# Kernel optimization log

Measured on AMD Instinct MI355X. Metric: run time of the kernel, lower is better.

## Reference

```python
import jax, jax.numpy as jnp
import numpy as np

EPS = 1e-6

def rmsnorm(x, w):
    # x: (B, N, D), w: (D,)
    var = jnp.mean(jnp.square(x), axis=-1, keepdims=True)
    return x * jax.lax.rsqrt(var + EPS) * w

def head_mixing(x):
    # Parameter-free cross-head mix: split each head's D dims into N chunks
    # and transpose the (head, chunk) axes. x: (B, N, D), D % N == 0.
    B, N, D = x.shape
    c = D // N
    return x.reshape(B, N, N, c).transpose(0, 2, 1, 3).reshape(B, N, D)

def setup_inputs() -> dict:
    key = jax.random.key(0)
    ks = jax.random.split(key, 4)
    B, N, D, H = 8192, 16, 256, 512
    return {
        "x": jax.random.normal(ks[0], (B, N, D), dtype=jnp.float32),
        "norm1_w": jnp.ones((D,), dtype=jnp.float32),
        "norm2_w": jnp.ones((D,), dtype=jnp.float32),
        "w1": jax.random.normal(ks[1], (N, D, H), dtype=jnp.float32) * (1.0 / np.sqrt(D)),
        "w3": jax.random.normal(ks[2], (N, D, H), dtype=jnp.float32) * (1.0 / np.sqrt(D)),
        "w2": jax.random.normal(ks[3], (N, H, D), dtype=jnp.float32) * (1.0 / np.sqrt(H)),
    }

def reference(x, norm1_w, norm2_w, w1, w3, w2):
    # P = HeadMixing(RMSNorm(X)) + X
    p = head_mixing(rmsnorm(x, norm1_w)) + x
    # Q = PerHeadSwiGLUFFN(RMSNorm(P)) + P  (grouped per-head SwiGLU)
    pn = rmsnorm(p, norm2_w)                       # (B, N, D)
    g = jnp.einsum('bnd,ndh->bnh', pn, w1)         # gate proj
    u = jnp.einsum('bnd,ndh->bnh', pn, w3)         # up proj
    h = jax.nn.silu(g) * u                         # (B, N, H)
    q = jnp.einsum('bnh,nhd->bnd', h, w2) + p
    return q
```

## Files before the change

kernel.cpp:

```cpp
#include <hip/hip_runtime.h>
#include <hip/hip_bf16.h>

#define B_ 8192
#define N_ 16
#define D_ 256
#define H_ 512

using bf16x8 = __attribute__((ext_vector_type(8))) short;
using f32x4  = __attribute__((ext_vector_type(4))) float;

__device__ __forceinline__ void gload_lds16(const void* g, void* l) {
    __builtin_amdgcn_global_load_lds(
        (const __attribute__((address_space(1))) void*)g,
        (__attribute__((address_space(3))) void*)l, 16, 0, 0);
}

__device__ __forceinline__ short f2bf(float f) {
    unsigned int u = __float_as_uint(f);
    u += 0x7fffu + ((u >> 16) & 1u);
    return (short)(u >> 16);
}

__device__ __forceinline__ float bf2f(short s) {
    return __uint_as_float(((unsigned int)(unsigned short)s) << 16);
}

__device__ __forceinline__ unsigned int pack2(float lo, float hi) {
    return (unsigned int)(unsigned short)f2bf(lo)
         | ((unsigned int)(unsigned short)f2bf(hi) << 16);
}

__device__ __forceinline__ f32x4 mfma(bf16x8 a, bf16x8 b, f32x4 c) {
    return __builtin_amdgcn_mfma_f32_16x16x32_bf16(a, b, c, 0, 0, 0);
}

__device__ __forceinline__ bf16x8 rd64(const short* base, int row, int g) {
    int gp = (g ^ row) & 7;
    return *(const bf16x8*)&base[(row << 6) + (gp << 3)];
}

template<int NT, int SA, int SB>
__device__ __forceinline__ void gemmc(const short* __restrict__ Ag,
                                      const short* __restrict__ Bg,
                                      short* As, short* Bs,
                                      f32x4 (&acc)[4][4],
                                      int t, int rowA0, int rowB0) {
    int lane = t & 63;
    int l16 = lane & 15, kq = lane >> 4;
    int srow = t >> 3;
    int sg   = ((t & 7) ^ srow) & 7;
    const short* Asrc = Ag + (size_t)srow * SA + sg * 8;
    const short* Bsrc = Bg + (size_t)srow * SB + sg * 8;

#pragma unroll
    for (int kt = 0; kt < NT; ++kt) {
        const int k0 = kt * 64;
#pragma unroll
        for (int rnd = 0; rnd < 4; ++rnd)
            gload_lds16(Asrc + rnd * 32 * SA + k0, As + rnd * 2048 + t * 8);
#pragma unroll
        for (int rnd = 0; rnd < 4; ++rnd)
            gload_lds16(Bsrc + rnd * 32 * SB + k0, Bs + rnd * 2048 + t * 8);
        __syncthreads();

#pragma unroll
        for (int kh = 0; kh < 2; ++kh) {
            int g = kh * 4 + kq;
            bf16x8 aF[4], bF[4];
#pragma unroll
            for (int j = 0; j < 4; ++j)
                bF[j] = rd64(Bs, rowB0 + j * 16 + l16, g);
#pragma unroll
            for (int i = 0; i < 4; ++i)
                aF[i] = rd64(As, rowA0 + i * 16 + l16, g);
#pragma unroll
            for (int i = 0; i < 4; ++i)
#pragma unroll
                for (int j = 0; j < 4; ++j)
                    acc[i][j] = mfma(aF[i], bF[j], acc[i][j]);
        }
        __syncthreads();
    }
}

__global__ __launch_bounds__(256) void k_prep(const float* __restrict__ w1,
                                              const float* __restrict__ w3,
                                              const float* __restrict__ w2,
                                              short* __restrict__ wgu,
                                              short* __restrict__ w2t) {
    int o = blockIdx.x * 256 + threadIdx.x;
    int n = o >> 17;
    int r = o & 131071;
    int h = r >> 8, d = r & 255;
    size_t base = ((size_t)n * 1024 + (h >> 4) * 32 + (h & 15)) * 256 + d;
    wgu[base]            = f2bf(w1[(size_t)n * 131072 + (size_t)d * 512 + h]);
    wgu[base + 16 * 256] = f2bf(w3[(size_t)n * 131072 + (size_t)d * 512 + h]);
    int d2 = r >> 9, h2 = r & 511;
    w2t[o] = f2bf(w2[(size_t)n * 131072 + (size_t)h2 * 256 + d2]);
}

__global__ __launch_bounds__(256) void k_mix(const float* __restrict__ x,
                                             const float* __restrict__ n1w,
                                             const float* __restrict__ n2w,
                                             unsigned int* __restrict__ pb_u,
                                             unsigned int* __restrict__ pn_u) {
    __shared__ __align__(16) float xs[N_ * D_];
    __shared__ __align__(16) float ps[N_ * D_];
    __shared__ float inv1[N_];
    __shared__ float inv2[N_];
    int b = blockIdx.x;
    int t = threadIdx.x;
    int w = t >> 6, lane = t & 63;

    const float4* xb4 = (const float4*)(x + (size_t)b * (N_ * D_));
    float4* xs4 = (float4*)xs;
    float4* ps4 = (float4*)ps;
#pragma unroll
    for (int i = 0; i < 4; ++i) xs4[t + i * 256] = xb4[t + i * 256];
    __syncthreads();

#pragma unroll
    for (int q = 0; q < 4; ++q) {
        int row = w * 4 + q;
        float4 v = xs4[row * 64 + lane];
        float s = v.x * v.x + v.y * v.y + v.z * v.z + v.w * v.w;
        s += __shfl_xor(s, 1);  s += __shfl_xor(s, 2);
        s += __shfl_xor(s, 4);  s += __shfl_xor(s, 8);
        s += __shfl_xor(s, 16); s += __shfl_xor(s, 32);
        if (lane == 0) inv1[row] = rsqrtf(s * (1.0f / 256.0f) + 1e-6f);
    }
    __syncthreads();

    {
        int n = t >> 4, j = t & 15;
        float i1 = inv1[n];
#pragma unroll 1
        for (int m = 0; m < 16; ++m) {
            int mm = (m + n) & 15;
            float v = xs[n * 256 + mm * 16 + j] * i1 * n1w[mm * 16 + j]
                    + xs[mm * 256 + t];
            ps[mm * 256 + t] = v;
        }
    }
    __syncthreads();

#pragma unroll
    for (int q = 0; q < 4; ++q) {
        int row = w * 4 + q;
        float4 v = ps4[row * 64 + lane];
        float s = v.x * v.x + v.y * v.y + v.z * v.z + v.w * v.w;
        s += __shfl_xor(s, 1);  s += __shfl_xor(s, 2);
        s += __shfl_xor(s, 4);  s += __shfl_xor(s, 8);
        s += __shfl_xor(s, 16); s += __shfl_xor(s, 32);
        if (lane == 0) inv2[row] = rsqrtf(s * (1.0f / 256.0f) + 1e-6f);
    }
    __syncthreads();

    int dh = t & 127, mh = t >> 7;
    float wA = n2w[2 * dh], wB = n2w[2 * dh + 1];
#pragma unroll
    for (int i = 0; i < 8; ++i) {
        int m = mh * 8 + i;
        float2 f = *(const float2*)&ps[m * 256 + 2 * dh];
        float iv = inv2[m];
        size_t off = ((size_t)m * B_ + b) * (D_ / 2) + dh;
        pb_u[off] = pack2(f.x, f.y);
        pn_u[off] = pack2(f.x * iv * wA, f.y * iv * wB);
    }
}

__global__ __launch_bounds__(256, 4) void k_gu(const short* __restrict__ pn,
                                               const short* __restrict__ wgu,
                                               short* __restrict__ hact) {
    __shared__ __align__(16) short As[128 * 64];
    __shared__ __align__(16) short Bs[128 * 64];

    int bid = blockIdx.x;
    int bx = (bid & 7) * 1024 + (bid >> 3);
    int head = bx >> 9;
    int mt = (bx >> 3) & 63;
    int nt = bx & 7;

    int t = threadIdx.x;
    int w = t >> 6, lane = t & 63;
    int l16 = lane & 15, kq = lane >> 4;
    int wm = w >> 1, wn = w & 1;

    f32x4 acc[4][4];
#pragma unroll
    for (int i = 0; i < 4; ++i)
#pragma unroll
        for (int j = 0; j < 4; ++j) acc[i][j] = (f32x4){0.f, 0.f, 0.f, 0.f};

    const short* Ag = pn  + ((size_t)head * B_ + (size_t)mt * 128) * D_;
    const short* Bg = wgu + ((size_t)head * 1024 + (size_t)nt * 128) * D_;

    gemmc<4, 256, 256>(Ag, Bg, As, Bs, acc, t, wm * 64, wn * 64);

    size_t hb = (size_t)head * B_ * H_;
#pragma unroll
    for (int mf = 0; mf < 4; ++mf) {
        int m = mt * 128 + wm * 64 + mf * 16 + kq * 4;
#pragma unroll
        for (int p = 0; p < 2; ++p) {
            int h = nt * 64 + (wn * 2 + p) * 16 + l16;
#pragma unroll
            for (int r = 0; r < 4; ++r) {
                float g = acc[mf][2 * p][r];
                float u = acc[mf][2 * p + 1][r];
                float hv = g * (1.0f / (1.0f + __expf(-g))) * u;
                hact[hb + (size_t)(m + r) * H_ + h] = f2bf(hv);
            }
        }
    }
}

__global__ __launch_bounds__(256, 4) void k_dn(const short* __restrict__ hact,
                                               const short* __restrict__ w2t,
                                               const short* __restrict__ pb,
                                               float* __restrict__ out) {
    __shared__ __align__(16) short As[128 * 64];
    __shared__ __align__(16) short Bs[128 * 64];

    int bid = blockIdx.x;
    int bx = (bid & 7) * 256 + (bid >> 3);
    int head = bx >> 7;
    int mt = (bx >> 1) & 63;
    int nt = bx & 1;

    int t = threadIdx.x;
    int w = t >> 6, lane = t & 63;
    int l16 = lane & 15, kq = lane >> 4;
    int wm = w >> 1, wn = w & 1;

    f32x4 acc[4][4];
#pragma unroll
    for (int i = 0; i < 4; ++i)
#pragma unroll
        for (int j = 0; j < 4; ++j) acc[i][j] = (f32x4){0.f, 0.f, 0.f, 0.f};

    const short* Ag = hact + ((size_t)head * B_ + (size_t)mt * 128) * H_;
    const short* Bg = w2t  + ((size_t)head * D_ + (size_t)nt * 128) * H_;

    gemmc<8, 512, 512>(Ag, Bg, As, Bs, acc, t, wm * 64, wn * 64);

#pragma unroll
    for (int mf = 0; mf < 4; ++mf) {
        int m = mt * 128 + wm * 64 + mf * 16 + kq * 4;
#pragma unroll
        for (int nf = 0; nf < 4; ++nf) {
            int d = nt * 128 + wn * 64 + nf * 16 + l16;
#pragma unroll
            for (int r = 0; r < 4; ++r) {
                float v = acc[mf][nf][r]
                        + bf2f(pb[((size_t)head * B_ + m + r) * D_ + d]);
                out[(size_t)(m + r) * (N_ * D_) + head * D_ + d] = v;
            }
        }
    }
}

extern "C" void kernel_launch(void* const* d_in, const int* in_sizes, int n_in,
                              void* d_out, int out_size, void* d_ws, size_t ws_size,
                              hipStream_t stream) {
    const float* x   = (const float*)d_in[0];
    const float* n1w = (const float*)d_in[1];
    const float* n2w = (const float*)d_in[2];
    const float* w1  = (const float*)d_in[3];
    const float* w3  = (const float*)d_in[4];
    const float* w2  = (const float*)d_in[5];
    float* out = (float*)d_out;

    char* ws = (char*)d_ws;
    short* wgu  = (short*)(ws);
    short* w2t  = (short*)(ws + (8ull   << 20));
    short* pn   = (short*)(ws + (12ull  << 20));
    short* pb   = (short*)(ws + (76ull  << 20));
    short* hact = (short*)(ws + (140ull << 20));

    k_prep<<<(N_ * D_ * H_) / 256, 256, 0, stream>>>(w1, w3, w2, wgu, w2t);
    k_mix<<<B_, 256, 0, stream>>>(x, n1w, n2w,
                                  (unsigned int*)pb, (unsigned int*)pn);
    k_gu<<<N_ * (B_ / 128) * (1024 / 128), 256, 0, stream>>>(pn, wgu, hact);
    k_dn<<<N_ * (B_ / 128) * (D_ / 128), 256, 0, stream>>>(hact, w2t, pb, out);
}
```

Before: 289.7 us.

## Use 256x256 tiles with 8 waves and double-buffered LDS prefetch in GEMMs

Replaces the 128x128, 4-wave GEMM core with a 256x256, 8-wave (512-thread) tile whose A/B panels are double-buffered in 128 KB of dynamic LDS. The next k-slice is staged in four phases interleaved with MFMA work, using explicit waitcnt/barriers and s_setprio. The goal is to hide global-load latency and raise arithmetic intensity per tile. In exchange it reduces occupancy to one block per CU, uses more accumulator registers, and launches fewer blocks in total, which may leave the final wave of blocks unevenly spread across CUs.

```diff
diff --git a/kernel.cpp b/kernel.cpp
--- a/kernel.cpp
+++ b/kernel.cpp
@@ -34,52 +34,103 @@
     return __builtin_amdgcn_mfma_f32_16x16x32_bf16(a, b, c, 0, 0, 0);
 }
 
-__device__ __forceinline__ bf16x8 rd64(const short* base, int row, int g) {
+__device__ __forceinline__ bf16x8 rdp(const short* base, int row, int g) {
     int gp = (g ^ row) & 7;
     return *(const bf16x8*)&base[(row << 6) + (gp << 3)];
 }
 
+template<int S>
+__device__ __forceinline__ void stage_half(const short* __restrict__ gsrc,
+                                           int k0, short* panel, int half,
+                                           int t) {
+#pragma unroll
+    for (int rnd = 0; rnd < 2; ++rnd) {
+        int flat = half * 1024 + rnd * 512 + t;
+        int row = flat >> 3, g = flat & 7;
+        int sg = (g ^ row) & 7;
+        gload_lds16(gsrc + (size_t)row * S + k0 + sg * 8, panel + flat * 8);
+    }
+}
+
+#define WAIT_VM0   do { asm volatile("s_waitcnt vmcnt(0)" ::: "memory");   \
+                        __builtin_amdgcn_sched_barrier(0); } while (0)
+#define WAIT_LGKM0 do { asm volatile("s_waitcnt lgkmcnt(0)" ::: "memory"); \
+                        __builtin_amdgcn_sched_barrier(0); } while (0)
+#define BARRIER    do { __builtin_amdgcn_sched_barrier(0);                 \
+                        asm volatile("s_barrier" ::: "memory");            \
+                        __builtin_amdgcn_sched_barrier(0); } while (0)
+
 template<int NT, int SA, int SB>
-__device__ __forceinline__ void gemmc(const short* __restrict__ Ag,
-                                      const short* __restrict__ Bg,
-                                      short* As, short* Bs,
-                                      f32x4 (&acc)[4][4],
-                                      int t, int rowA0, int rowB0) {
+__device__ __forceinline__ void gemm8p(const short* __restrict__ Ag,
+                                       const short* __restrict__ Bg,
+                                       short* sm, f32x4 (&acc)[8][4],
+                                       int t) {
     int lane = t & 63;
     int l16 = lane & 15, kq = lane >> 4;
-    int srow = t >> 3;
-    int sg   = ((t & 7) ^ srow) & 7;
-    const short* Asrc = Ag + (size_t)srow * SA + sg * 8;
-    const short* Bsrc = Bg + (size_t)srow * SB + sg * 8;
-
-#pragma unroll
+    int w = t >> 6;
+    int rowA0 = (w >> 2) * 128;
+    int rowB0 = (w & 3) * 64;
+
+    stage_half<SA>(Ag, 0, sm, 0, t);
+    stage_half<SA>(Ag, 0, sm, 1, t);
+    stage_half<SB>(Bg, 0, sm + 32768, 0, t);
+    stage_half<SB>(Bg, 0, sm + 32768, 1, t);
+    WAIT_VM0;
+    BARRIER;
+
+#pragma unroll 1
     for (int kt = 0; kt < NT; ++kt) {
-        const int k0 = kt * 64;
-#pragma unroll
-        for (int rnd = 0; rnd < 4; ++rnd)
-            gload_lds16(Asrc + rnd * 32 * SA + k0, As + rnd * 2048 + t * 8);
-#pragma unroll
-        for (int rnd = 0; rnd < 4; ++rnd)
-            gload_lds16(Bsrc + rnd * 32 * SB + k0, Bs + rnd * 2048 + t * 8);
-        __syncthreads();
-
-#pragma unroll
-        for (int kh = 0; kh < 2; ++kh) {
-            int g = kh * 4 + kq;
-            bf16x8 aF[4], bF[4];
-#pragma unroll
-            for (int j = 0; j < 4; ++j)
-                bF[j] = rd64(Bs, rowB0 + j * 16 + l16, g);
-#pragma unroll
-            for (int i = 0; i < 4; ++i)
-                aF[i] = rd64(As, rowA0 + i * 16 + l16, g);
-#pragma unroll
-            for (int i = 0; i < 4; ++i)
-#pragma unroll
-                for (int j = 0; j < 4; ++j)
-                    acc[i][j] = mfma(aF[i], bF[j], acc[i][j]);
+        short* As  = sm + (kt & 1) * 16384;
+        short* Bs  = sm + 32768 + (kt & 1) * 16384;
+        short* Asn = sm + ((kt + 1) & 1) * 16384;
+        short* Bsn = sm + 32768 + ((kt + 1) & 1) * 16384;
+        const bool pf = (kt + 1) < NT;
+        const int kn = (kt + 1) * 64;
+
+        bf16x8 aF[4][2], bF[2][2];
+
+#define PHASE(MH, NH, STAGE_STMT)                                          \
+    do {                                                                   \
+        if (NH == 0) {                                                     \
+            _Pragma("unroll")                                              \
+            for (int i = 0; i < 4; ++i)                                    \
+                _Pragma("unroll")                                          \
+                for (int kh = 0; kh < 2; ++kh)                             \
+                    aF[i][kh] = rdp(As, rowA0 + (MH) * 64 + i * 16 + l16,  \
+                                    kh * 4 + kq);                          \
+        }                                                                  \
+        _Pragma("unroll")                                                  \
+        for (int j = 0; j < 2; ++j)                                        \
+            _Pragma("unroll")                                              \
+            for (int kh = 0; kh < 2; ++kh)                                 \
+                bF[j][kh] = rdp(Bs, rowB0 + (NH) * 32 + j * 16 + l16,      \
+                                kh * 4 + kq);                              \
+        STAGE_STMT;                                                        \
+        WAIT_LGKM0;                                                        \
+        __builtin_amdgcn_s_setprio(1);                                     \
+        _Pragma("unroll")                                                  \
+        for (int i = 0; i < 4; ++i)                                        \
+            _Pragma("unroll")                                              \
+            for (int j = 0; j < 2; ++j)                                    \
+                _Pragma("unroll")                                          \
+                for (int kh = 0; kh < 2; ++kh)                             \
+                    acc[(MH) * 4 + i][(NH) * 2 + j] =                      \
+                        mfma(aF[i][kh], bF[j][kh],                         \
+                             acc[(MH) * 4 + i][(NH) * 2 + j]);             \
+        __builtin_amdgcn_s_setprio(0);                                     \
+        BARRIER;                                                           \
+    } while (0)
+
+        PHASE(0, 0, if (pf) stage_half<SA>(Ag, kn, Asn, 0, t));
+        PHASE(0, 1, if (pf) stage_half<SA>(Ag, kn, Asn, 1, t));
+        PHASE(1, 0, if (pf) stage_half<SB>(Bg, kn, Bsn, 0, t));
+        PHASE(1, 1, if (pf) stage_half<SB>(Bg, kn, Bsn, 1, t));
+#undef PHASE
+
+        if (pf) {
+            WAIT_VM0;
+            BARRIER;
         }
-        __syncthreads();
     }
 }
 
@@ -169,41 +220,40 @@
     }
 }
 
-__global__ __launch_bounds__(256, 4) void k_gu(const short* __restrict__ pn,
+__global__ __launch_bounds__(512, 2) void k_gu(const short* __restrict__ pn,
                                                const short* __restrict__ wgu,
                                                short* __restrict__ hact) {
-    __shared__ __align__(16) short As[128 * 64];
-    __shared__ __align__(16) short Bs[128 * 64];
+    extern __shared__ short sm[];
 
     int bid = blockIdx.x;
-    int bx = (bid & 7) * 1024 + (bid >> 3);
-    int head = bx >> 9;
-    int mt = (bx >> 3) & 63;
-    int nt = bx & 7;
+    int bx = (bid & 7) * 256 + (bid >> 3);
+    int head = bx >> 7;
+    int mt = (bx >> 2) & 31;
+    int nt = bx & 3;
 
     int t = threadIdx.x;
-    int w = t >> 6, lane = t & 63;
+    int lane = t & 63, w = t >> 6;
     int l16 = lane & 15, kq = lane >> 4;
-    int wm = w >> 1, wn = w & 1;
-
-    f32x4 acc[4][4];
-#pragma unroll
-    for (int i = 0; i < 4; ++i)
+    int wm = w >> 2, wn = w & 3;
+
+    f32x4 acc[8][4];
+#pragma unroll
+    for (int i = 0; i < 8; ++i)
 #pragma unroll
         for (int j = 0; j < 4; ++j) acc[i][j] = (f32x4){0.f, 0.f, 0.f, 0.f};
 
-    const short* Ag = pn  + ((size_t)head * B_ + (size_t)mt * 128) * D_;
-    const short* Bg = wgu + ((size_t)head * 1024 + (size_t)nt * 128) * D_;
-
-    gemmc<4, 256, 256>(Ag, Bg, As, Bs, acc, t, wm * 64, wn * 64);
+    const short* Ag = pn  + ((size_t)head * B_ + (size_t)mt * 256) * D_;
+    const short* Bg = wgu + ((size_t)head * 1024 + (size_t)nt * 256) * D_;
+
+    gemm8p<4, D_, D_>(Ag, Bg, sm, acc, t);
 
     size_t hb = (size_t)head * B_ * H_;
 #pragma unroll
-    for (int mf = 0; mf < 4; ++mf) {
-        int m = mt * 128 + wm * 64 + mf * 16 + kq * 4;
+    for (int mf = 0; mf < 8; ++mf) {
+        int m = mt * 256 + wm * 128 + mf * 16 + kq * 4;
 #pragma unroll
         for (int p = 0; p < 2; ++p) {
-            int h = nt * 64 + (wn * 2 + p) * 16 + l16;
+            int h = (nt * 8 + wn * 2 + p) * 16 + l16;
 #pragma unroll
             for (int r = 0; r < 4; ++r) {
                 float g = acc[mf][2 * p][r];
@@ -215,41 +265,39 @@
     }
 }
 
-__global__ __launch_bounds__(256, 4) void k_dn(const short* __restrict__ hact,
+__global__ __launch_bounds__(512, 2) void k_dn(const short* __restrict__ hact,
                                                const short* __restrict__ w2t,
                                                const short* __restrict__ pb,
                                                float* __restrict__ out) {
-    __shared__ __align__(16) short As[128 * 64];
-    __shared__ __align__(16) short Bs[128 * 64];
+    extern __shared__ short sm[];
 
     int bid = blockIdx.x;
-    int bx = (bid & 7) * 256 + (bid >> 3);
-    int head = bx >> 7;
-    int mt = (bx >> 1) & 63;
-    int nt = bx & 1;
+    int bx = (bid & 7) * 64 + (bid >> 3);
+    int head = bx >> 5;
+    int mt = bx & 31;
 
     int t = threadIdx.x;
-    int w = t >> 6, lane = t & 63;
+    int lane = t & 63, w = t >> 6;
     int l16 = lane & 15, kq = lane >> 4;
-    int wm = w >> 1, wn = w & 1;
-
-    f32x4 acc[4][4];
-#pragma unroll
-    for (int i = 0; i < 4; ++i)
+    int wm = w >> 2, wn = w & 3;
+
+    f32x4 acc[8][4];
+#pragma unroll
+    for (int i = 0; i < 8; ++i)
 #pragma unroll
         for (int j = 0; j < 4; ++j) acc[i][j] = (f32x4){0.f, 0.f, 0.f, 0.f};
 
-    const short* Ag = hact + ((size_t)head * B_ + (size_t)mt * 128) * H_;
-    const short* Bg = w2t  + ((size_t)head * D_ + (size_t)nt * 128) * H_;
-
-    gemmc<8, 512, 512>(Ag, Bg, As, Bs, acc, t, wm * 64, wn * 64);
-
-#pragma unroll
-    for (int mf = 0; mf < 4; ++mf) {
-        int m = mt * 128 + wm * 64 + mf * 16 + kq * 4;
+    const short* Ag = hact + ((size_t)head * B_ + (size_t)mt * 256) * H_;
+    const short* Bg = w2t  + (size_t)head * D_ * H_;
+
+    gemm8p<8, H_, H_>(Ag, Bg, sm, acc, t);
+
+#pragma unroll
+    for (int mf = 0; mf < 8; ++mf) {
+        int m = mt * 256 + wm * 128 + mf * 16 + kq * 4;
 #pragma unroll
         for (int nf = 0; nf < 4; ++nf) {
-            int d = nt * 128 + wn * 64 + nf * 16 + l16;
+            int d = wn * 64 + nf * 16 + l16;
 #pragma unroll
             for (int r = 0; r < 4; ++r) {
                 float v = acc[mf][nf][r]
@@ -278,9 +326,14 @@
     short* pb   = (short*)(ws + (76ull  << 20));
     short* hact = (short*)(ws + (140ull << 20));
 
+    (void)hipFuncSetAttribute((const void*)k_gu,
+                              hipFuncAttributeMaxDynamicSharedMemorySize, 131072);
+    (void)hipFuncSetAttribute((const void*)k_dn,
+                              hipFuncAttributeMaxDynamicSharedMemorySize, 131072);
+
     k_prep<<<(N_ * D_ * H_) / 256, 256, 0, stream>>>(w1, w3, w2, wgu, w2t);
     k_mix<<<B_, 256, 0, stream>>>(x, n1w, n2w,
                                   (unsigned int*)pb, (unsigned int*)pn);
-    k_gu<<<N_ * (B_ / 128) * (1024 / 128), 256, 0, stream>>>(pn, wgu, hact);
-    k_dn<<<N_ * (B_ / 128) * (D_ / 128), 256, 0, stream>>>(hact, w2t, pb, out);
-}
+    k_gu<<<N_ * (B_ / 256) * 4, 512, 131072, stream>>>(pn, wgu, hact);
+    k_dn<<<N_ * (B_ / 256), 512, 131072, stream>>>(hact, w2t, pb, out);
+}
```

Result: slower. 309.3 us (+6.8%).
